# Kernel tuning notes

Measured on AMD Instinct MI355X. Metric: run time of the kernel, lower is better.

The kernel has to match this reference:

```python
import jax, jax.numpy as jnp
import numpy as np

M = 8192          # tokens
DIM = 2048        # per-stream width; K = 4*DIM
S = 4             # fixed stream count (Stream4 kernels)
N = 32            # fixed GEMM output width
SINKHORN_ITERS = 20


def setup_inputs() -> dict:
    key = jax.random.key(0)
    k1, k2 = jax.random.split(key)
    X = jax.random.normal(k1, (M, S * DIM), dtype=jnp.float32)
    # scale W so H = X @ W is O(1): keeps sigmoid/exp/sinkhorn numerically sane
    W = jax.random.normal(k2, (S * DIM, N), dtype=jnp.float32) / np.float32(np.sqrt(S * DIM))
    # module init: beta = zeros(24), alpha = ones(3), concatenated
    alpha_beta = jnp.concatenate([jnp.zeros(24, jnp.float32), jnp.ones(3, jnp.float32)])
    return {"X": X, "W": W, "alpha_beta": alpha_beta}


def _sinkhorn(P, iters=SINKHORN_ITERS):
    # doubly-stochastic normalization of [M, S, S] matrices
    for _ in range(iters):
        P = P / jnp.sum(P, axis=-1, keepdims=True)  # row normalize
        P = P / jnp.sum(P, axis=-2, keepdims=True)  # col normalize
    return P


def reference(X, W, alpha_beta):
    Mm, K = X.shape
    d = K // S
    # skinny GEMM producing the mixing logits (fused w/ SplitK in the kernel)
    H = X @ W                                   # [M, 32]
    b_res, b_pre, b_pos = alpha_beta[0:16], alpha_beta[16:20], alpha_beta[20:24]
    a_res, a_pre, a_pos = alpha_beta[24], alpha_beta[25], alpha_beta[26]
    H_pre = a_pre * jax.nn.sigmoid(H[:, 16:20]) + b_pre          # [M, 4]
    H_pos = a_pos * jax.nn.sigmoid(H[:, 20:24]) + b_pos          # [M, 4]
    H_res = (a_res * H[:, 0:16] + b_res).reshape(Mm, S, S)       # [M, 4, 4]
    H_res = _sinkhorn(jnp.exp(H_res))                            # doubly stochastic
    # view X as 4 streams of width d
    Xs = X.reshape(Mm, S, d)                                     # [M, 4, d]
    # ApplyPreTransform: collapse streams with H_pre weights
    Y = jnp.einsum('ms,msd->md', H_pre, Xs)                      # [M, d]
    # ApplyResidual: per-token 4x4 stream mix + broadcast of pre-transformed feature
    O = jnp.einsum('msi,mid->msd', H_res, Xs) + H_pos[:, :, None] * Y[:, None, :]
    return O.reshape(Mm, K)
```

## Files before the change

### kernel.cpp

```cpp
#include <hip/hip_runtime.h>
#include <math.h>
#include <stdint.h>

#define K_DIM 8192
#define D_DIM 2048
#define M_ROWS 8192
#define N_W 32
#define NC 24
#define KSPLIT 8
#define KRANGE (K_DIM / KSPLIT)
#define NKSTEP (KRANGE / 32)
#define TOTAL_KSTEPS (K_DIM / 32)

typedef short bf16x8 __attribute__((ext_vector_type(8)));
typedef float f32x4 __attribute__((ext_vector_type(4)));
union U32x4 { uint32_t u[4]; bf16x8 v; };

#define WFRAG_IDX(ks, tile, hilo) ((((ks) * 2 + (tile)) * 2 + (hilo)) * 64)

__global__ __launch_bounds__(256) void mhc_prepack_kernel(
    const float* __restrict__ W, unsigned short* __restrict__ wfrag,
    float* __restrict__ Hsum)
{
    const int idx = blockIdx.x * 256 + threadIdx.x;
    const int k = idx >> 5, n = idx & 31;
    const float w = W[(size_t)k * N_W + n];
    const uint32_t u = __float_as_uint(w);
    const float hif = __uint_as_float(u & 0xFFFF0000u);
    const uint32_t ur = __float_as_uint(w - hif);

    const int ks = k >> 5, kk = k & 31;
    const int lane = ((kk >> 3) << 4) | (n & 15);
    const int e = kk & 7;
    const int tile = n >> 4;
    unsigned short* p = wfrag + ((size_t)WFRAG_IDX(ks, tile, 0) + lane) * 8 + e;
    p[0]   = (unsigned short)(u >> 16);
    p[512] = (unsigned short)(ur >> 16);

    if (idx < M_ROWS * NC) Hsum[idx] = 0.f;
}

__global__ __launch_bounds__(256) void mhc_gemm_kernel(
    const float* __restrict__ X, const unsigned short* __restrict__ wfrag,
    float* __restrict__ Hsum)
{
    const int t = threadIdx.x;
    const int l = t & 63;
    const int wv = t >> 6;
    const int rowbase = blockIdx.x * 64;
    const int ks0 = blockIdx.y * NKSTEP;

    f32x4 c0 = {0.f, 0.f, 0.f, 0.f};
    f32x4 c1 = {0.f, 0.f, 0.f, 0.f};

    const int arow = rowbase + wv * 16 + (l & 15);
    const float* __restrict__ xrow = X + (size_t)arow * K_DIM + ((l >> 4) * 8);
    const bf16x8* __restrict__ wf = reinterpret_cast<const bf16x8*>(wfrag);

#pragma unroll 2
    for (int s = 0; s < NKSTEP; ++s) {
        const int ks = ks0 + s;
        const float* xc = xrow + ks * 32;
        const float4 xa = *reinterpret_cast<const float4*>(xc);
        const float4 xb = *reinterpret_cast<const float4*>(xc + 4);
        float xs[8];
        xs[0] = xa.x; xs[1] = xa.y; xs[2] = xa.z; xs[3] = xa.w;
        xs[4] = xb.x; xs[5] = xb.y; xs[6] = xb.z; xs[7] = xb.w;

        U32x4 ah, al;
#pragma unroll
        for (int p = 0; p < 4; ++p) {
            const uint32_t u0 = __float_as_uint(xs[2 * p]);
            const uint32_t u1 = __float_as_uint(xs[2 * p + 1]);
            const float h0 = __uint_as_float(u0 & 0xFFFF0000u);
            const float h1 = __uint_as_float(u1 & 0xFFFF0000u);
            const uint32_t r0 = __float_as_uint(xs[2 * p] - h0);
            const uint32_t r1 = __float_as_uint(xs[2 * p + 1] - h1);
            ah.u[p] = (u1 & 0xFFFF0000u) | (u0 >> 16);
            al.u[p] = (r1 & 0xFFFF0000u) | (r0 >> 16);
        }

        const bf16x8 bh0 = wf[WFRAG_IDX(ks, 0, 0) + l];
        const bf16x8 bl0 = wf[WFRAG_IDX(ks, 0, 1) + l];
        const bf16x8 bh1 = wf[WFRAG_IDX(ks, 1, 0) + l];
        const bf16x8 bl1 = wf[WFRAG_IDX(ks, 1, 1) + l];

        c0 = __builtin_amdgcn_mfma_f32_16x16x32_bf16(ah.v, bh0, c0, 0, 0, 0);
        c0 = __builtin_amdgcn_mfma_f32_16x16x32_bf16(al.v, bh0, c0, 0, 0, 0);
        c0 = __builtin_amdgcn_mfma_f32_16x16x32_bf16(ah.v, bl0, c0, 0, 0, 0);
        c1 = __builtin_amdgcn_mfma_f32_16x16x32_bf16(ah.v, bh1, c1, 0, 0, 0);
        c1 = __builtin_amdgcn_mfma_f32_16x16x32_bf16(al.v, bh1, c1, 0, 0, 0);
        c1 = __builtin_amdgcn_mfma_f32_16x16x32_bf16(ah.v, bl1, c1, 0, 0, 0);
    }

    const int drow = rowbase + wv * 16 + (l >> 4) * 4;
    const int col = l & 15;
#pragma unroll
    for (int r = 0; r < 4; ++r)
        atomicAdd(&Hsum[(size_t)(drow + r) * NC + col], c0[r]);
    if (col < 8) {
#pragma unroll
        for (int r = 0; r < 4; ++r)
            atomicAdd(&Hsum[(size_t)(drow + r) * NC + 16 + col], c1[r]);
    }
}

__global__ __launch_bounds__(256) void mhc_apply_kernel(
    const float* __restrict__ X, const float* __restrict__ Hsum,
    const float* __restrict__ ab, float* __restrict__ out)
{
    __shared__ float pbuf[NC];
    const int row = blockIdx.x;
    const int t = threadIdx.x;

    if (t < 64) {
        const int lane = t;
        const float pl = (lane < NC) ? Hsum[(size_t)row * NC + lane] : 0.f;
        const float bias  = (lane < NC) ? ab[lane] : 0.f;
        const float scale = ab[(lane < 16) ? 24 : ((lane < 20) ? 25 : 26)];

        float vout;
        if (lane < 16) {
            vout = __expf(fmaf(scale, pl, bias));
        } else {
            vout = fmaf(scale, 1.f / (1.f + __expf(-pl)), bias);
        }

        float p = vout;
        for (int it = 0; it < 20; ++it) {
            float rs = p + __shfl_xor(p, 1);
            rs += __shfl_xor(rs, 2);
            p = p / rs;
            float cs = p + __shfl_xor(p, 4);
            cs += __shfl_xor(cs, 8);
            p = p / cs;
        }
        if (lane < NC) pbuf[lane] = (lane < 16) ? p : vout;
    }
    __syncthreads();

    float hres[4][4], hpre[4], hpos[4];
#pragma unroll
    for (int i = 0; i < 16; ++i) hres[i >> 2][i & 3] = pbuf[i];
#pragma unroll
    for (int i = 0; i < 4; ++i) hpre[i] = pbuf[16 + i];
#pragma unroll
    for (int i = 0; i < 4; ++i) hpos[i] = pbuf[20 + i];

    const float4* __restrict__ Xr =
        reinterpret_cast<const float4*>(X + (size_t)row * K_DIM);
    float4* __restrict__ Or = reinterpret_cast<float4*>(out + (size_t)row * K_DIM);

#pragma unroll
    for (int q = 0; q < 2; ++q) {
        const int pos = t + q * 256;
        float4 xq[4];
#pragma unroll
        for (int i = 0; i < 4; ++i) xq[i] = Xr[i * (D_DIM / 4) + pos];

        float y[4];
#pragma unroll
        for (int e = 0; e < 4; ++e) {
            float s = 0.f;
#pragma unroll
            for (int i = 0; i < 4; ++i)
                s = fmaf(hpre[i], reinterpret_cast<const float*>(&xq[i])[e], s);
            y[e] = s;
        }

#pragma unroll
        for (int s = 0; s < 4; ++s) {
            float4 o;
            float* oe = reinterpret_cast<float*>(&o);
#pragma unroll
            for (int e = 0; e < 4; ++e) {
                float v = hpos[s] * y[e];
#pragma unroll
                for (int i = 0; i < 4; ++i)
                    v = fmaf(hres[s][i], reinterpret_cast<const float*>(&xq[i])[e], v);
                oe[e] = v;
            }
            Or[s * (D_DIM / 4) + pos] = o;
        }
    }
}

extern "C" void kernel_launch(void* const* d_in, const int* in_sizes, int n_in,
                              void* d_out, int out_size, void* d_ws, size_t ws_size,
                              hipStream_t stream) {
    const float* X  = (const float*)d_in[0];
    const float* W  = (const float*)d_in[1];
    const float* ab = (const float*)d_in[2];
    float* out = (float*)d_out;
    float* Hsum = (float*)d_ws;
    unsigned short* wfrag = (unsigned short*)((char*)d_ws + (size_t)M_ROWS * NC * 4);

    mhc_prepack_kernel<<<(K_DIM * N_W) / 256, 256, 0, stream>>>(W, wfrag, Hsum);
    dim3 g1(M_ROWS / 64, KSPLIT);
    mhc_gemm_kernel<<<g1, 256, 0, stream>>>(X, wfrag, Hsum);
    mhc_apply_kernel<<<M_ROWS, 256, 0, stream>>>(X, Hsum, ab, out);
}
```

Before: 183.4 us.

## Fuse skinny GEMM, Sinkhorn and residual apply into one row-block kernel

Replaces the split-K GEMM (with atomics into a workspace) and the separate apply kernel with one fused kernel. Each 512-thread block handles 4 rows. It keeps those rows of X in registers, stages them through LDS to feed the MFMA, reduces partial sums across waves in shared memory, runs Sinkhorn and then writes the output from the registers. The goal is to read X from HBM once instead of twice and to drop the atomics, the Hsum zeroing and one launch. The cost is that every block now reads the whole prepacked W fragment buffer, which adds a lot of L2 traffic. MFMA rows are also mostly duplicated, since only 4 of 16 are distinct.

```diff
diff --git a/kernel.cpp b/kernel.cpp
--- a/kernel.cpp
+++ b/kernel.cpp
@@ -7,9 +7,8 @@
 #define M_ROWS 8192
 #define N_W 32
 #define NC 24
-#define KSPLIT 8
-#define KRANGE (K_DIM / KSPLIT)
-#define NKSTEP (KRANGE / 32)
+#define RB 4
+#define THREADS 512
 #define TOTAL_KSTEPS (K_DIM / 32)
 
 typedef short bf16x8 __attribute__((ext_vector_type(8)));
@@ -19,8 +18,7 @@
 #define WFRAG_IDX(ks, tile, hilo) ((((ks) * 2 + (tile)) * 2 + (hilo)) * 64)
 
 __global__ __launch_bounds__(256) void mhc_prepack_kernel(
-    const float* __restrict__ W, unsigned short* __restrict__ wfrag,
-    float* __restrict__ Hsum)
+    const float* __restrict__ W, unsigned short* __restrict__ wfrag)
 {
     const int idx = blockIdx.x * 256 + threadIdx.x;
     const int k = idx >> 5, n = idx & 31;
@@ -36,97 +34,106 @@
     unsigned short* p = wfrag + ((size_t)WFRAG_IDX(ks, tile, 0) + lane) * 8 + e;
     p[0]   = (unsigned short)(u >> 16);
     p[512] = (unsigned short)(ur >> 16);
-
-    if (idx < M_ROWS * NC) Hsum[idx] = 0.f;
 }
 
-__global__ __launch_bounds__(256) void mhc_gemm_kernel(
+__global__ __launch_bounds__(THREADS, 4) void mhc_fused_kernel(
     const float* __restrict__ X, const unsigned short* __restrict__ wfrag,
-    float* __restrict__ Hsum)
+    const float* __restrict__ ab, float* __restrict__ out)
 {
+    __shared__ __align__(16) float Xl[RB * D_DIM];
+    __shared__ float Hpart[8][RB][NC];
+    __shared__ float pbuf[RB][NC];
+
     const int t = threadIdx.x;
     const int l = t & 63;
     const int wv = t >> 6;
-    const int rowbase = blockIdx.x * 64;
-    const int ks0 = blockIdx.y * NKSTEP;
+    const int rowbase = blockIdx.x * RB;
+
+    const float4* __restrict__ Xg = reinterpret_cast<const float4*>(X);
+    float4 x4[RB][4];
+#pragma unroll
+    for (int i = 0; i < 4; ++i)
+#pragma unroll
+        for (int r = 0; r < RB; ++r)
+            x4[r][i] = Xg[(size_t)(rowbase + r) * (K_DIM / 4) + i * 512 + t];
 
     f32x4 c0 = {0.f, 0.f, 0.f, 0.f};
     f32x4 c1 = {0.f, 0.f, 0.f, 0.f};
-
-    const int arow = rowbase + wv * 16 + (l & 15);
-    const float* __restrict__ xrow = X + (size_t)arow * K_DIM + ((l >> 4) * 8);
     const bf16x8* __restrict__ wf = reinterpret_cast<const bf16x8*>(wfrag);
-
-#pragma unroll 2
-    for (int s = 0; s < NKSTEP; ++s) {
-        const int ks = ks0 + s;
-        const float* xc = xrow + ks * 32;
-        const float4 xa = *reinterpret_cast<const float4*>(xc);
-        const float4 xb = *reinterpret_cast<const float4*>(xc + 4);
-        float xs[8];
-        xs[0] = xa.x; xs[1] = xa.y; xs[2] = xa.z; xs[3] = xa.w;
-        xs[4] = xb.x; xs[5] = xb.y; xs[6] = xb.z; xs[7] = xb.w;
-
-        U32x4 ah, al;
-#pragma unroll
-        for (int p = 0; p < 4; ++p) {
-            const uint32_t u0 = __float_as_uint(xs[2 * p]);
-            const uint32_t u1 = __float_as_uint(xs[2 * p + 1]);
-            const float h0 = __uint_as_float(u0 & 0xFFFF0000u);
-            const float h1 = __uint_as_float(u1 & 0xFFFF0000u);
-            const uint32_t r0 = __float_as_uint(xs[2 * p] - h0);
-            const uint32_t r1 = __float_as_uint(xs[2 * p + 1] - h1);
-            ah.u[p] = (u1 & 0xFFFF0000u) | (u0 >> 16);
-            al.u[p] = (r1 & 0xFFFF0000u) | (r0 >> 16);
-        }
-
-        const bf16x8 bh0 = wf[WFRAG_IDX(ks, 0, 0) + l];
-        const bf16x8 bl0 = wf[WFRAG_IDX(ks, 0, 1) + l];
-        const bf16x8 bh1 = wf[WFRAG_IDX(ks, 1, 0) + l];
-        const bf16x8 bl1 = wf[WFRAG_IDX(ks, 1, 1) + l];
-
-        c0 = __builtin_amdgcn_mfma_f32_16x16x32_bf16(ah.v, bh0, c0, 0, 0, 0);
-        c0 = __builtin_amdgcn_mfma_f32_16x16x32_bf16(al.v, bh0, c0, 0, 0, 0);
-        c0 = __builtin_amdgcn_mfma_f32_16x16x32_bf16(ah.v, bl0, c0, 0, 0, 0);
-        c1 = __builtin_amdgcn_mfma_f32_16x16x32_bf16(ah.v, bh1, c1, 0, 0, 0);
-        c1 = __builtin_amdgcn_mfma_f32_16x16x32_bf16(al.v, bh1, c1, 0, 0, 0);
-        c1 = __builtin_amdgcn_mfma_f32_16x16x32_bf16(ah.v, bl1, c1, 0, 0, 0);
-    }
-
-    const int drow = rowbase + wv * 16 + (l >> 4) * 4;
-    const int col = l & 15;
-#pragma unroll
-    for (int r = 0; r < 4; ++r)
-        atomicAdd(&Hsum[(size_t)(drow + r) * NC + col], c0[r]);
-    if (col < 8) {
-#pragma unroll
-        for (int r = 0; r < 4; ++r)
-            atomicAdd(&Hsum[(size_t)(drow + r) * NC + 16 + col], c1[r]);
-    }
-}
-
-__global__ __launch_bounds__(256) void mhc_apply_kernel(
-    const float* __restrict__ X, const float* __restrict__ Hsum,
-    const float* __restrict__ ab, float* __restrict__ out)
-{
-    __shared__ float pbuf[NC];
-    const int row = blockIdx.x;
-    const int t = threadIdx.x;
-
-    if (t < 64) {
-        const int lane = t;
-        const float pl = (lane < NC) ? Hsum[(size_t)row * NC + lane] : 0.f;
-        const float bias  = (lane < NC) ? ab[lane] : 0.f;
-        const float scale = ab[(lane < 16) ? 24 : ((lane < 20) ? 25 : 26)];
-
-        float vout;
-        if (lane < 16) {
-            vout = __expf(fmaf(scale, pl, bias));
-        } else {
-            vout = fmaf(scale, 1.f / (1.f + __expf(-pl)), bias);
-        }
-
-        float p = vout;
+    const int abase = (l & 3) * D_DIM + ((l >> 4) << 3);
+
+#pragma unroll
+    for (int i = 0; i < 4; ++i) {
+        if (i) __syncthreads();
+#pragma unroll
+        for (int r = 0; r < RB; ++r)
+            *reinterpret_cast<float4*>(&Xl[r * D_DIM + (t << 2)]) = x4[r][i];
+        __syncthreads();
+
+#pragma unroll
+        for (int s = 0; s < 8; ++s) {
+            const int ksl = wv * 8 + s;
+            const int ks = i * 64 + ksl;
+            const float* xp = &Xl[abase + ksl * 32];
+            const float4 xa = *reinterpret_cast<const float4*>(xp);
+            const float4 xb = *reinterpret_cast<const float4*>(xp + 4);
+            float xs[8];
+            xs[0] = xa.x; xs[1] = xa.y; xs[2] = xa.z; xs[3] = xa.w;
+            xs[4] = xb.x; xs[5] = xb.y; xs[6] = xb.z; xs[7] = xb.w;
+
+            U32x4 ah, al;
+#pragma unroll
+            for (int p = 0; p < 4; ++p) {
+                const uint32_t u0 = __float_as_uint(xs[2 * p]);
+                const uint32_t u1 = __float_as_uint(xs[2 * p + 1]);
+                const float h0 = __uint_as_float(u0 & 0xFFFF0000u);
+                const float h1 = __uint_as_float(u1 & 0xFFFF0000u);
+                const uint32_t r0 = __float_as_uint(xs[2 * p] - h0);
+                const uint32_t r1 = __float_as_uint(xs[2 * p + 1] - h1);
+                ah.u[p] = (u1 & 0xFFFF0000u) | (u0 >> 16);
+                al.u[p] = (r1 & 0xFFFF0000u) | (r0 >> 16);
+            }
+
+            const bf16x8 bh0 = wf[WFRAG_IDX(ks, 0, 0) + l];
+            const bf16x8 bl0 = wf[WFRAG_IDX(ks, 0, 1) + l];
+            const bf16x8 bh1 = wf[WFRAG_IDX(ks, 1, 0) + l];
+            const bf16x8 bl1 = wf[WFRAG_IDX(ks, 1, 1) + l];
+
+            c0 = __builtin_amdgcn_mfma_f32_16x16x32_bf16(ah.v, bh0, c0, 0, 0, 0);
+            c0 = __builtin_amdgcn_mfma_f32_16x16x32_bf16(al.v, bh0, c0, 0, 0, 0);
+            c0 = __builtin_amdgcn_mfma_f32_16x16x32_bf16(ah.v, bl0, c0, 0, 0, 0);
+            c1 = __builtin_amdgcn_mfma_f32_16x16x32_bf16(ah.v, bh1, c1, 0, 0, 0);
+            c1 = __builtin_amdgcn_mfma_f32_16x16x32_bf16(al.v, bh1, c1, 0, 0, 0);
+            c1 = __builtin_amdgcn_mfma_f32_16x16x32_bf16(ah.v, bl1, c1, 0, 0, 0);
+        }
+    }
+
+    __syncthreads();
+    if (l < 16) {
+#pragma unroll
+        for (int r = 0; r < RB; ++r) Hpart[wv][r][l] = c0[r];
+    }
+    if (l < 8) {
+#pragma unroll
+        for (int r = 0; r < RB; ++r) Hpart[wv][r][16 + l] = c1[r];
+    }
+    __syncthreads();
+
+    if (wv == 0) {
+        float h0 = 0.f;
+#pragma unroll
+        for (int w = 0; w < 8; ++w) h0 += Hpart[w][l >> 4][l & 15];
+        float p = __expf(fmaf(ab[24], h0, ab[l & 15]));
+
+        if (l < 32) {
+            float h1 = 0.f;
+#pragma unroll
+            for (int w = 0; w < 8; ++w) h1 += Hpart[w][l >> 3][16 + (l & 7)];
+            const int ci = 16 + (l & 7);
+            const float sc = (ci < 20) ? ab[25] : ab[26];
+            pbuf[l >> 3][ci] = fmaf(sc, 1.f / (1.f + __expf(-h1)), ab[ci]);
+        }
+
         for (int it = 0; it < 20; ++it) {
             float rs = p + __shfl_xor(p, 1);
             rs += __shfl_xor(rs, 2);
@@ -135,52 +142,46 @@
             cs += __shfl_xor(cs, 8);
             p = p / cs;
         }
-        if (lane < NC) pbuf[lane] = (lane < 16) ? p : vout;
+        pbuf[l >> 4][l & 15] = p;
     }
     __syncthreads();
 
-    float hres[4][4], hpre[4], hpos[4];
-#pragma unroll
-    for (int i = 0; i < 16; ++i) hres[i >> 2][i & 3] = pbuf[i];
-#pragma unroll
-    for (int i = 0; i < 4; ++i) hpre[i] = pbuf[16 + i];
-#pragma unroll
-    for (int i = 0; i < 4; ++i) hpos[i] = pbuf[20 + i];
-
-    const float4* __restrict__ Xr =
-        reinterpret_cast<const float4*>(X + (size_t)row * K_DIM);
-    float4* __restrict__ Or = reinterpret_cast<float4*>(out + (size_t)row * K_DIM);
-
-#pragma unroll
-    for (int q = 0; q < 2; ++q) {
-        const int pos = t + q * 256;
-        float4 xq[4];
-#pragma unroll
-        for (int i = 0; i < 4; ++i) xq[i] = Xr[i * (D_DIM / 4) + pos];
+    float4* __restrict__ Og = reinterpret_cast<float4*>(out);
+#pragma unroll
+    for (int r = 0; r < RB; ++r) {
+        float hre[4][4], hpr[4], hpo[4];
+#pragma unroll
+        for (int q = 0; q < 16; ++q) hre[q >> 2][q & 3] = pbuf[r][q];
+#pragma unroll
+        for (int q = 0; q < 4; ++q) hpr[q] = pbuf[r][16 + q];
+#pragma unroll
+        for (int q = 0; q < 4; ++q) hpo[q] = pbuf[r][20 + q];
 
         float y[4];
 #pragma unroll
         for (int e = 0; e < 4; ++e) {
-            float s = 0.f;
+            float v = 0.f;
 #pragma unroll
             for (int i = 0; i < 4; ++i)
-                s = fmaf(hpre[i], reinterpret_cast<const float*>(&xq[i])[e], s);
-            y[e] = s;
-        }
-
+                v = fmaf(hpr[i], reinterpret_cast<const float*>(&x4[r][i])[e], v);
+            y[e] = v;
+        }
+
+        const size_t ob = (size_t)(rowbase + r) * (K_DIM / 4);
 #pragma unroll
         for (int s = 0; s < 4; ++s) {
             float4 o;
             float* oe = reinterpret_cast<float*>(&o);
 #pragma unroll
             for (int e = 0; e < 4; ++e) {
-                float v = hpos[s] * y[e];
+                float v = hpo[s] * y[e];
 #pragma unroll
                 for (int i = 0; i < 4; ++i)
-                    v = fmaf(hres[s][i], reinterpret_cast<const float*>(&xq[i])[e], v);
+                    v = fmaf(hre[s][i],
+                             reinterpret_cast<const float*>(&x4[r][i])[e], v);
                 oe[e] = v;
             }
-            Or[s * (D_DIM / 4) + pos] = o;
+            Og[ob + s * 512 + t] = o;
         }
     }
 }
@@ -192,11 +193,8 @@
     const float* W  = (const float*)d_in[1];
     const float* ab = (const float*)d_in[2];
     float* out = (float*)d_out;
-    float* Hsum = (float*)d_ws;
-    unsigned short* wfrag = (unsigned short*)((char*)d_ws + (size_t)M_ROWS * NC * 4);
-
-    mhc_prepack_kernel<<<(K_DIM * N_W) / 256, 256, 0, stream>>>(W, wfrag, Hsum);
-    dim3 g1(M_ROWS / 64, KSPLIT);
-    mhc_gemm_kernel<<<g1, 256, 0, stream>>>(X, wfrag, Hsum);
-    mhc_apply_kernel<<<M_ROWS, 256, 0, stream>>>(X, Hsum, ab, out);
+    unsigned short* wfrag = (unsigned short*)d_ws;
+
+    mhc_prepack_kernel<<<(K_DIM * N_W) / 256, 256, 0, stream>>>(W, wfrag);
+    mhc_fused_kernel<<<M_ROWS / RB, THREADS, 0, stream>>>(X, wfrag, ab, out);
 }
```

New measurement: 182.4 us. No clear change (-0.6%).

## Replace split-K atomic GEMM with LDS-staged full-K row blocks and in-block reduction

Applied to the files above, without the earlier changes.

The skinny GEMM no longer splits K across blocks with global atomics. Each 512-thread block now owns 16 rows over the full K. It stages X chunks through double-buffered padded LDS with coalesced loads prefetched into registers, and the 8 waves split the k-steps within each chunk. Partial results are reduced through shared memory and written once, which removes the atomics and the zero-init of Hsum. In exchange there are fewer, larger blocks (512), a sync per chunk and a large LDS footprint that may limit occupancy.

```diff
diff --git a/kernel.cpp b/kernel.cpp
--- a/kernel.cpp
+++ b/kernel.cpp
@@ -7,10 +7,12 @@
 #define M_ROWS 8192
 #define N_W 32
 #define NC 24
-#define KSPLIT 8
-#define KRANGE (K_DIM / KSPLIT)
-#define NKSTEP (KRANGE / 32)
-#define TOTAL_KSTEPS (K_DIM / 32)
+#define ROWS 16
+#define THREADS 512
+#define CHUNK_COLS 512
+#define NCHUNKS (K_DIM / CHUNK_COLS)
+#define PADF 516
+#define PAD4 (PADF / 4)
 
 typedef short bf16x8 __attribute__((ext_vector_type(8)));
 typedef float f32x4 __attribute__((ext_vector_type(4)));
@@ -19,8 +21,7 @@
 #define WFRAG_IDX(ks, tile, hilo) ((((ks) * 2 + (tile)) * 2 + (hilo)) * 64)
 
 __global__ __launch_bounds__(256) void mhc_prepack_kernel(
-    const float* __restrict__ W, unsigned short* __restrict__ wfrag,
-    float* __restrict__ Hsum)
+    const float* __restrict__ W, unsigned short* __restrict__ wfrag)
 {
     const int idx = blockIdx.x * 256 + threadIdx.x;
     const int k = idx >> 5, n = idx & 31;
@@ -36,72 +37,106 @@
     unsigned short* p = wfrag + ((size_t)WFRAG_IDX(ks, tile, 0) + lane) * 8 + e;
     p[0]   = (unsigned short)(u >> 16);
     p[512] = (unsigned short)(ur >> 16);
-
-    if (idx < M_ROWS * NC) Hsum[idx] = 0.f;
-}
-
-__global__ __launch_bounds__(256) void mhc_gemm_kernel(
+}
+
+__global__ __launch_bounds__(THREADS, 4) void mhc_gemm_kernel(
     const float* __restrict__ X, const unsigned short* __restrict__ wfrag,
     float* __restrict__ Hsum)
 {
+    __shared__ __align__(16) float Xl[2][ROWS * PADF];
+    __shared__ float Hpart[8][ROWS][NC];
     const int t = threadIdx.x;
     const int l = t & 63;
     const int wv = t >> 6;
-    const int rowbase = blockIdx.x * 64;
-    const int ks0 = blockIdx.y * NKSTEP;
+    const int rowbase = blockIdx.x * ROWS;
 
     f32x4 c0 = {0.f, 0.f, 0.f, 0.f};
     f32x4 c1 = {0.f, 0.f, 0.f, 0.f};
-
-    const int arow = rowbase + wv * 16 + (l & 15);
-    const float* __restrict__ xrow = X + (size_t)arow * K_DIM + ((l >> 4) * 8);
+    const float4* __restrict__ Xg = reinterpret_cast<const float4*>(X);
     const bf16x8* __restrict__ wf = reinterpret_cast<const bf16x8*>(wfrag);
 
-#pragma unroll 2
-    for (int s = 0; s < NKSTEP; ++s) {
-        const int ks = ks0 + s;
-        const float* xc = xrow + ks * 32;
-        const float4 xa = *reinterpret_cast<const float4*>(xc);
-        const float4 xb = *reinterpret_cast<const float4*>(xc + 4);
-        float xs[8];
-        xs[0] = xa.x; xs[1] = xa.y; xs[2] = xa.z; xs[3] = xa.w;
-        xs[4] = xb.x; xs[5] = xb.y; xs[6] = xb.z; xs[7] = xb.w;
-
-        U32x4 ah, al;
-#pragma unroll
-        for (int p = 0; p < 4; ++p) {
-            const uint32_t u0 = __float_as_uint(xs[2 * p]);
-            const uint32_t u1 = __float_as_uint(xs[2 * p + 1]);
-            const float h0 = __uint_as_float(u0 & 0xFFFF0000u);
-            const float h1 = __uint_as_float(u1 & 0xFFFF0000u);
-            const uint32_t r0 = __float_as_uint(xs[2 * p] - h0);
-            const uint32_t r1 = __float_as_uint(xs[2 * p + 1] - h1);
-            ah.u[p] = (u1 & 0xFFFF0000u) | (u0 >> 16);
-            al.u[p] = (r1 & 0xFFFF0000u) | (r0 >> 16);
-        }
-
-        const bf16x8 bh0 = wf[WFRAG_IDX(ks, 0, 0) + l];
-        const bf16x8 bl0 = wf[WFRAG_IDX(ks, 0, 1) + l];
-        const bf16x8 bh1 = wf[WFRAG_IDX(ks, 1, 0) + l];
-        const bf16x8 bl1 = wf[WFRAG_IDX(ks, 1, 1) + l];
-
-        c0 = __builtin_amdgcn_mfma_f32_16x16x32_bf16(ah.v, bh0, c0, 0, 0, 0);
-        c0 = __builtin_amdgcn_mfma_f32_16x16x32_bf16(al.v, bh0, c0, 0, 0, 0);
-        c0 = __builtin_amdgcn_mfma_f32_16x16x32_bf16(ah.v, bl0, c0, 0, 0, 0);
-        c1 = __builtin_amdgcn_mfma_f32_16x16x32_bf16(ah.v, bh1, c1, 0, 0, 0);
-        c1 = __builtin_amdgcn_mfma_f32_16x16x32_bf16(al.v, bh1, c1, 0, 0, 0);
-        c1 = __builtin_amdgcn_mfma_f32_16x16x32_bf16(ah.v, bl1, c1, 0, 0, 0);
-    }
-
-    const int drow = rowbase + wv * 16 + (l >> 4) * 4;
-    const int col = l & 15;
+    float4 pf[4];
+    auto LOADC = [&](int c) {
+#pragma unroll
+        for (int j = 0; j < 4; ++j) {
+            const int F = j * THREADS + t;
+            const int row = F >> 7, slot = F & 127;
+            pf[j] = Xg[(size_t)(rowbase + row) * (K_DIM / 4) + c * 128 + slot];
+        }
+    };
+    auto WRITEC = [&](int b) {
+        float4* dst = reinterpret_cast<float4*>(Xl[b]);
+#pragma unroll
+        for (int j = 0; j < 4; ++j) {
+            const int F = j * THREADS + t;
+            const int row = F >> 7, slot = F & 127;
+            dst[row * PAD4 + slot] = pf[j];
+        }
+    };
+
+    LOADC(0);
+    WRITEC(0);
+    __syncthreads();
+
+    for (int c = 0; c < NCHUNKS; ++c) {
+        if (c + 1 < NCHUNKS) LOADC(c + 1);
+        const float* xt = Xl[c & 1];
+#pragma unroll
+        for (int u = 0; u < 2; ++u) {
+            const int ksl = wv * 2 + u;
+            const int ks = c * 16 + ksl;
+            const float* xp = xt + (l & 15) * PADF + ksl * 32 + ((l >> 4) << 3);
+            const float4 xa = *reinterpret_cast<const float4*>(xp);
+            const float4 xb = *reinterpret_cast<const float4*>(xp + 4);
+            float xs[8];
+            xs[0] = xa.x; xs[1] = xa.y; xs[2] = xa.z; xs[3] = xa.w;
+            xs[4] = xb.x; xs[5] = xb.y; xs[6] = xb.z; xs[7] = xb.w;
+
+            U32x4 ah, al;
+#pragma unroll
+            for (int p = 0; p < 4; ++p) {
+                const uint32_t u0 = __float_as_uint(xs[2 * p]);
+                const uint32_t u1 = __float_as_uint(xs[2 * p + 1]);
+                const float h0 = __uint_as_float(u0 & 0xFFFF0000u);
+                const float h1 = __uint_as_float(u1 & 0xFFFF0000u);
+                const uint32_t r0 = __float_as_uint(xs[2 * p] - h0);
+                const uint32_t r1 = __float_as_uint(xs[2 * p + 1] - h1);
+                ah.u[p] = (u1 & 0xFFFF0000u) | (u0 >> 16);
+                al.u[p] = (r1 & 0xFFFF0000u) | (r0 >> 16);
+            }
+
+            const bf16x8 bh0 = wf[WFRAG_IDX(ks, 0, 0) + l];
+            const bf16x8 bl0 = wf[WFRAG_IDX(ks, 0, 1) + l];
+            const bf16x8 bh1 = wf[WFRAG_IDX(ks, 1, 0) + l];
+            const bf16x8 bl1 = wf[WFRAG_IDX(ks, 1, 1) + l];
+
+            c0 = __builtin_amdgcn_mfma_f32_16x16x32_bf16(ah.v, bh0, c0, 0, 0, 0);
+            c0 = __builtin_amdgcn_mfma_f32_16x16x32_bf16(al.v, bh0, c0, 0, 0, 0);
+            c0 = __builtin_amdgcn_mfma_f32_16x16x32_bf16(ah.v, bl0, c0, 0, 0, 0);
+            c1 = __builtin_amdgcn_mfma_f32_16x16x32_bf16(ah.v, bh1, c1, 0, 0, 0);
+            c1 = __builtin_amdgcn_mfma_f32_16x16x32_bf16(al.v, bh1, c1, 0, 0, 0);
+            c1 = __builtin_amdgcn_mfma_f32_16x16x32_bf16(ah.v, bl1, c1, 0, 0, 0);
+        }
+        if (c + 1 < NCHUNKS) WRITEC((c + 1) & 1);
+        __syncthreads();
+    }
+
 #pragma unroll
     for (int r = 0; r < 4; ++r)
-        atomicAdd(&Hsum[(size_t)(drow + r) * NC + col], c0[r]);
-    if (col < 8) {
+        Hpart[wv][((l >> 4) << 2) + r][l & 15] = c0[r];
+    if ((l & 15) < 8) {
 #pragma unroll
         for (int r = 0; r < 4; ++r)
-            atomicAdd(&Hsum[(size_t)(drow + r) * NC + 16 + col], c1[r]);
+            Hpart[wv][((l >> 4) << 2) + r][16 + (l & 15)] = c1[r];
+    }
+    __syncthreads();
+
+    if (t < ROWS * NC) {
+        const int row = t / NC, col = t % NC;
+        float h = 0.f;
+#pragma unroll
+        for (int w = 0; w < 8; ++w) h += Hpart[w][row][col];
+        Hsum[(size_t)(rowbase + row) * NC + col] = h;
     }
 }
 
@@ -192,11 +227,10 @@
     const float* W  = (const float*)d_in[1];
     const float* ab = (const float*)d_in[2];
     float* out = (float*)d_out;
-    float* Hsum = (float*)d_ws;
-    unsigned short* wfrag = (unsigned short*)((char*)d_ws + (size_t)M_ROWS * NC * 4);
-
-    mhc_prepack_kernel<<<(K_DIM * N_W) / 256, 256, 0, stream>>>(W, wfrag, Hsum);
-    dim3 g1(M_ROWS / 64, KSPLIT);
-    mhc_gemm_kernel<<<g1, 256, 0, stream>>>(X, wfrag, Hsum);
+    unsigned short* wfrag = (unsigned short*)d_ws;
+    float* Hsum = (float*)((char*)d_ws + 1048576);
+
+    mhc_prepack_kernel<<<(K_DIM * N_W) / 256, 256, 0, stream>>>(W, wfrag);
+    mhc_gemm_kernel<<<M_ROWS / ROWS, THREADS, 0, stream>>>(X, wfrag, Hsum);
     mhc_apply_kernel<<<M_ROWS, 256, 0, stream>>>(X, Hsum, ab, out);
 }
```

Result: slower. 216.3 us (+17.9%).

## Stage W fragments in LDS and raise split-K to 32 with 128-row blocks

Applied to the files above, without the earlier changes.

The GEMM now splits K 32 ways and gives each block 128 rows. Each block copies its slice of the prepacked bf16 W fragments into shared memory once and reuses them across the two 16-row tiles each wave handles. This replaces the per-step global W fragment loads and gives a larger grid. In exchange it issues four times as many atomicAdds into Hsum, and the workspace layout moves so the W fragments come first.

```diff
diff --git a/kernel.cpp b/kernel.cpp
--- a/kernel.cpp
+++ b/kernel.cpp
@@ -7,10 +7,11 @@
 #define M_ROWS 8192
 #define N_W 32
 #define NC 24
-#define KSPLIT 8
+#define KSPLIT 32
 #define KRANGE (K_DIM / KSPLIT)
-#define NKSTEP (KRANGE / 32)
-#define TOTAL_KSTEPS (K_DIM / 32)
+#define KSB 8
+#define RPB 128
+#define THREADS 256
 
 typedef short bf16x8 __attribute__((ext_vector_type(8)));
 typedef float f32x4 __attribute__((ext_vector_type(4)));
@@ -40,68 +41,81 @@
     if (idx < M_ROWS * NC) Hsum[idx] = 0.f;
 }
 
-__global__ __launch_bounds__(256) void mhc_gemm_kernel(
+__global__ __launch_bounds__(THREADS, 4) void mhc_gemm_kernel(
     const float* __restrict__ X, const unsigned short* __restrict__ wfrag,
     float* __restrict__ Hsum)
 {
+    __shared__ __align__(16) unsigned short bfr[KSB][2][2][64][8];
     const int t = threadIdx.x;
     const int l = t & 63;
     const int wv = t >> 6;
-    const int rowbase = blockIdx.x * 64;
-    const int ks0 = blockIdx.y * NKSTEP;
-
-    f32x4 c0 = {0.f, 0.f, 0.f, 0.f};
-    f32x4 c1 = {0.f, 0.f, 0.f, 0.f};
-
-    const int arow = rowbase + wv * 16 + (l & 15);
-    const float* __restrict__ xrow = X + (size_t)arow * K_DIM + ((l >> 4) * 8);
-    const bf16x8* __restrict__ wf = reinterpret_cast<const bf16x8*>(wfrag);
-
-#pragma unroll 2
-    for (int s = 0; s < NKSTEP; ++s) {
-        const int ks = ks0 + s;
-        const float* xc = xrow + ks * 32;
-        const float4 xa = *reinterpret_cast<const float4*>(xc);
-        const float4 xb = *reinterpret_cast<const float4*>(xc + 4);
-        float xs[8];
-        xs[0] = xa.x; xs[1] = xa.y; xs[2] = xa.z; xs[3] = xa.w;
-        xs[4] = xb.x; xs[5] = xb.y; xs[6] = xb.z; xs[7] = xb.w;
-
-        U32x4 ah, al;
-#pragma unroll
-        for (int p = 0; p < 4; ++p) {
-            const uint32_t u0 = __float_as_uint(xs[2 * p]);
-            const uint32_t u1 = __float_as_uint(xs[2 * p + 1]);
-            const float h0 = __uint_as_float(u0 & 0xFFFF0000u);
-            const float h1 = __uint_as_float(u1 & 0xFFFF0000u);
-            const uint32_t r0 = __float_as_uint(xs[2 * p] - h0);
-            const uint32_t r1 = __float_as_uint(xs[2 * p + 1] - h1);
-            ah.u[p] = (u1 & 0xFFFF0000u) | (u0 >> 16);
-            al.u[p] = (r1 & 0xFFFF0000u) | (r0 >> 16);
-        }
-
-        const bf16x8 bh0 = wf[WFRAG_IDX(ks, 0, 0) + l];
-        const bf16x8 bl0 = wf[WFRAG_IDX(ks, 0, 1) + l];
-        const bf16x8 bh1 = wf[WFRAG_IDX(ks, 1, 0) + l];
-        const bf16x8 bl1 = wf[WFRAG_IDX(ks, 1, 1) + l];
-
-        c0 = __builtin_amdgcn_mfma_f32_16x16x32_bf16(ah.v, bh0, c0, 0, 0, 0);
-        c0 = __builtin_amdgcn_mfma_f32_16x16x32_bf16(al.v, bh0, c0, 0, 0, 0);
-        c0 = __builtin_amdgcn_mfma_f32_16x16x32_bf16(ah.v, bl0, c0, 0, 0, 0);
-        c1 = __builtin_amdgcn_mfma_f32_16x16x32_bf16(ah.v, bh1, c1, 0, 0, 0);
-        c1 = __builtin_amdgcn_mfma_f32_16x16x32_bf16(al.v, bh1, c1, 0, 0, 0);
-        c1 = __builtin_amdgcn_mfma_f32_16x16x32_bf16(ah.v, bl1, c1, 0, 0, 0);
-    }
-
-    const int drow = rowbase + wv * 16 + (l >> 4) * 4;
-    const int col = l & 15;
-#pragma unroll
-    for (int r = 0; r < 4; ++r)
-        atomicAdd(&Hsum[(size_t)(drow + r) * NC + col], c0[r]);
-    if (col < 8) {
+    const int rowbase = blockIdx.x * RPB;
+    const int kbase = blockIdx.y * KRANGE;
+
+    {
+        const float4* __restrict__ src = reinterpret_cast<const float4*>(
+            wfrag + (size_t)blockIdx.y * (KSB * 2 * 2 * 64 * 8));
+        float4* dst = reinterpret_cast<float4*>(&bfr[0][0][0][0][0]);
+#pragma unroll
+        for (int q = 0; q < 8; ++q)
+            dst[q * THREADS + t] = src[q * THREADS + t];
+    }
+    __syncthreads();
+
+#pragma unroll
+    for (int tt = 0; tt < 2; ++tt) {
+        const int tile16 = wv + tt * 4;
+        const int arow = rowbase + tile16 * 16 + (l & 15);
+        const float* __restrict__ xp =
+            X + (size_t)arow * K_DIM + kbase + ((l >> 4) << 3);
+
+        f32x4 c0 = {0.f, 0.f, 0.f, 0.f};
+        f32x4 c1 = {0.f, 0.f, 0.f, 0.f};
+
+#pragma unroll
+        for (int s = 0; s < KSB; ++s) {
+            const float4 xa = *reinterpret_cast<const float4*>(xp + s * 32);
+            const float4 xb = *reinterpret_cast<const float4*>(xp + s * 32 + 4);
+            float xs[8];
+            xs[0] = xa.x; xs[1] = xa.y; xs[2] = xa.z; xs[3] = xa.w;
+            xs[4] = xb.x; xs[5] = xb.y; xs[6] = xb.z; xs[7] = xb.w;
+
+            U32x4 ah, al;
+#pragma unroll
+            for (int p = 0; p < 4; ++p) {
+                const uint32_t u0 = __float_as_uint(xs[2 * p]);
+                const uint32_t u1 = __float_as_uint(xs[2 * p + 1]);
+                const float h0 = __uint_as_float(u0 & 0xFFFF0000u);
+                const float h1 = __uint_as_float(u1 & 0xFFFF0000u);
+                const uint32_t r0 = __float_as_uint(xs[2 * p] - h0);
+                const uint32_t r1 = __float_as_uint(xs[2 * p + 1] - h1);
+                ah.u[p] = (u1 & 0xFFFF0000u) | (u0 >> 16);
+                al.u[p] = (r1 & 0xFFFF0000u) | (r0 >> 16);
+            }
+
+            const bf16x8 bh0 = *reinterpret_cast<const bf16x8*>(&bfr[s][0][0][l][0]);
+            const bf16x8 bl0 = *reinterpret_cast<const bf16x8*>(&bfr[s][0][1][l][0]);
+            const bf16x8 bh1 = *reinterpret_cast<const bf16x8*>(&bfr[s][1][0][l][0]);
+            const bf16x8 bl1 = *reinterpret_cast<const bf16x8*>(&bfr[s][1][1][l][0]);
+
+            c0 = __builtin_amdgcn_mfma_f32_16x16x32_bf16(ah.v, bh0, c0, 0, 0, 0);
+            c0 = __builtin_amdgcn_mfma_f32_16x16x32_bf16(al.v, bh0, c0, 0, 0, 0);
+            c0 = __builtin_amdgcn_mfma_f32_16x16x32_bf16(ah.v, bl0, c0, 0, 0, 0);
+            c1 = __builtin_amdgcn_mfma_f32_16x16x32_bf16(ah.v, bh1, c1, 0, 0, 0);
+            c1 = __builtin_amdgcn_mfma_f32_16x16x32_bf16(al.v, bh1, c1, 0, 0, 0);
+            c1 = __builtin_amdgcn_mfma_f32_16x16x32_bf16(ah.v, bl1, c1, 0, 0, 0);
+        }
+
+        const int drow = rowbase + tile16 * 16 + ((l >> 4) << 2);
+        const int col = l & 15;
 #pragma unroll
         for (int r = 0; r < 4; ++r)
-            atomicAdd(&Hsum[(size_t)(drow + r) * NC + 16 + col], c1[r]);
+            atomicAdd(&Hsum[(size_t)(drow + r) * NC + col], c0[r]);
+        if (col < 8) {
+#pragma unroll
+            for (int r = 0; r < 4; ++r)
+                atomicAdd(&Hsum[(size_t)(drow + r) * NC + 16 + col], c1[r]);
+        }
     }
 }
 
@@ -192,11 +206,11 @@
     const float* W  = (const float*)d_in[1];
     const float* ab = (const float*)d_in[2];
     float* out = (float*)d_out;
-    float* Hsum = (float*)d_ws;
-    unsigned short* wfrag = (unsigned short*)((char*)d_ws + (size_t)M_ROWS * NC * 4);
+    unsigned short* wfrag = (unsigned short*)d_ws;
+    float* Hsum = (float*)((char*)d_ws + 1048576);
 
     mhc_prepack_kernel<<<(K_DIM * N_W) / 256, 256, 0, stream>>>(W, wfrag, Hsum);
-    dim3 g1(M_ROWS / 64, KSPLIT);
-    mhc_gemm_kernel<<<g1, 256, 0, stream>>>(X, wfrag, Hsum);
+    dim3 g1(M_ROWS / RPB, KSPLIT);
+    mhc_gemm_kernel<<<g1, THREADS, 0, stream>>>(X, wfrag, Hsum);
     mhc_apply_kernel<<<M_ROWS, 256, 0, stream>>>(X, Hsum, ab, out);
 }
```

After: 193.2 us. +5.3%, slower.
